# Optimization experiments

Hardware: AMD Instinct MI355X
Metric: run time of the kernel (lower is better)

## Reference

```python
import jax, jax.numpy as jnp
import numpy as np

B, S, D = 2, 2048, 1024
H, HD = 16, 64
WIN = 256


def setup_inputs() -> dict:
    key = jax.random.key(0)
    ks = jax.random.split(key, 9)
    scale = 0.02
    x = jax.random.normal(ks[0], (B, S, D), dtype=jnp.float32)
    Wq = jax.random.normal(ks[1], (D, H * HD), dtype=jnp.float32) * scale
    Wk = jax.random.normal(ks[2], (D, H * HD), dtype=jnp.float32) * scale
    Wv = jax.random.normal(ks[3], (D, H * HD), dtype=jnp.float32) * scale
    Wo = jax.random.normal(ks[4], (H * HD, D), dtype=jnp.float32) * scale
    bq = jnp.zeros((H * HD,), jnp.float32)
    bk = jnp.zeros((H * HD,), jnp.float32)
    bv = jnp.zeros((H * HD,), jnp.float32)
    bo = jnp.zeros((D,), jnp.float32)
    return {"x": x, "Wq": Wq, "bq": bq, "Wk": Wk, "bk": bk,
            "Wv": Wv, "bv": bv, "Wo": Wo, "bo": bo}


def _band_mask(seq_len, window):
    # True where attention is DISALLOWED (matches torch masked positions).
    # mask=None in the original => prefix_size=0, row i attends to
    # j in [max(0, i - window), i]  (causal sliding window).
    i = jnp.arange(seq_len)[:, None]
    j = jnp.arange(seq_len)[None, :]
    return (j > i) | (j < i - window)


def reference(x, Wq, bq, Wk, bk, Wv, bv, Wo, bo):
    b, s, _ = x.shape
    q = (x @ Wq + bq).reshape(b, s, H, HD)
    k = (x @ Wk + bk).reshape(b, s, H, HD)
    v = (x @ Wv + bv).reshape(b, s, H, HD)
    scores = jnp.einsum("bihd,bjhd->bhij", q, k) / jnp.sqrt(jnp.float32(HD))
    mask = _band_mask(s, WIN)  # [s, s], broadcasts over batch, heads
    scores = jnp.where(mask[None, None, :, :], -jnp.inf, scores)
    attn = jax.nn.softmax(scores, axis=-1)  # dropout is identity at eval
    out = jnp.einsum("bhij,bjhd->bihd", attn, v).reshape(b, s, H * HD)
    return out @ Wo + bo
```

## Files before the change

### kernel.cpp

```cpp
#include <hip/hip_runtime.h>
#include <stdint.h>
#include <stddef.h>

#define S_LEN 2048
#define DMODEL 1024
#define NHEAD 16
#define HDIM 64
#define WINSZ 256
#define MROWS 4096
#define NQKV 3072

typedef __bf16 bf16x8 __attribute__((ext_vector_type(8)));
typedef float f32x4 __attribute__((ext_vector_type(4)));
typedef unsigned short us4 __attribute__((ext_vector_type(4)));
typedef unsigned short us8 __attribute__((ext_vector_type(8)));

#define MFMA16(a, b, c) __builtin_amdgcn_mfma_f32_16x16x32_bf16((a), (b), (c), 0, 0, 0)

__device__ __forceinline__ unsigned short f2b(float f) {
  union { float f; unsigned u; } v; v.f = f;
  unsigned u = v.u;
  unsigned r = (u + 0x7FFFu + ((u >> 16) & 1u)) >> 16;
  return (unsigned short)r;
}
__device__ __forceinline__ void storev(float* p, float v) { *p = v; }
__device__ __forceinline__ void storev(unsigned short* p, float v) { *p = f2b(v); }

__device__ __forceinline__ void gload_lds16(const unsigned short* g, unsigned short* l) {
  __builtin_amdgcn_global_load_lds(
      (const __attribute__((address_space(1))) unsigned int*)g,
      (__attribute__((address_space(3))) unsigned int*)l, 16, 0, 0);
}


__global__ void prep_kernel(const float* __restrict__ x,
                            const float* __restrict__ Wq, const float* __restrict__ Wk,
                            const float* __restrict__ Wv, const float* __restrict__ Wo,
                            const float* __restrict__ bq, const float* __restrict__ bk,
                            const float* __restrict__ bv,
                            unsigned short* __restrict__ xb, unsigned short* __restrict__ WqkvT,
                            unsigned short* __restrict__ WoT, float* __restrict__ bqkv) {
  __shared__ float tile[32][33];
  const int bid = blockIdx.x;
  const int tid = threadIdx.x;
  if (bid < 4096) {
    int i = (bid * 256 + tid) * 4;
    float4 v = *reinterpret_cast<const float4*>(x + i);
    us4 o;
    o[0] = f2b(v.x); o[1] = f2b(v.y); o[2] = f2b(v.z); o[3] = f2b(v.w);
    *reinterpret_cast<us4*>(xb + i) = o;
  } else if (bid < 8192) {
    int z = (bid - 4096) >> 10;
    int rem = (bid - 4096) & 1023;
    int bx = rem & 31, by = rem >> 5;
    const float* W = (z == 0) ? Wq : (z == 1) ? Wk : (z == 2) ? Wv : Wo;
    unsigned short* Wt = (z == 3) ? WoT : WqkvT + (size_t)z * DMODEL * DMODEL;
    int n0 = bx * 32, k0 = by * 32;
    int tx = tid & 31, ty = tid >> 5;
#pragma unroll
    for (int i = 0; i < 32; i += 8)
      tile[ty + i][tx] = W[(size_t)(k0 + ty + i) * DMODEL + n0 + tx];
    __syncthreads();
#pragma unroll
    for (int i = 0; i < 32; i += 8)
      Wt[(size_t)(n0 + ty + i) * DMODEL + k0 + tx] = f2b(tile[tx][ty + i]);
  } else {
    int i = (bid - 8192) * 256 + tid;
    if (i < DMODEL) {
      bqkv[i] = bq[i];
      bqkv[DMODEL + i] = bk[i];
      bqkv[2 * DMODEL + i] = bv[i];
    }
  }
}


__global__ __launch_bounds__(512, 2) void gemm8p_kernel(
    const unsigned short* __restrict__ A, const unsigned short* __restrict__ Bt,
    const float* __restrict__ bias, unsigned short* __restrict__ C, int N, int K) {
  __shared__ unsigned short As[2 * 2 * 128 * 64];
  __shared__ unsigned short Bs[2 * 3 * 64 * 64];
  const int tid = threadIdx.x;
  const int cpx = gridDim.x >> 3;
  const int nid = (blockIdx.x & 7) * cpx + (blockIdx.x >> 3);
  const int nbx = N / 192;
  const int by = nid / nbx, bx = nid - by * nbx;
  const int m0 = by * 256, n0 = bx * 192;
  const int wid = tid >> 6, l = tid & 63;
  const int wm = wid >> 2, wn = wid & 3;
  const int lr = l & 15, lg = l >> 4;
  const int srow = tid >> 3;
  const int scol = (tid & 7) * 8;
  const int scol_g = scol ^ (((tid >> 5) & 1) << 4);
  const int NT = K >> 6;

  f32x4 acc[8][3];
#pragma unroll
  for (int i = 0; i < 8; i++)
#pragma unroll
    for (int j = 0; j < 3; j++) acc[i][j] = (f32x4){0.f, 0.f, 0.f, 0.f};

  auto stA = [&](int q, int h, int kt) {
#pragma unroll
    for (int r = 0; r < 2; r++)
      gload_lds16(A + (size_t)(m0 + h * 128 + r * 64 + srow) * K + kt * 64 + scol_g,
                  &As[(((q * 2 + h) * 2 + r) * 64 + srow) * 64 + scol]);
  };
  auto stB = [&](int q, int c, int kt) {
    gload_lds16(Bt + (size_t)(n0 + c * 64 + srow) * K + kt * 64 + scol_g,
                &Bs[((q * 3 + c) * 64 + srow) * 64 + scol]);
  };

  stB(0, 0, 0); stB(0, 1, 0); stB(0, 2, 0); stA(0, 0, 0); stA(0, 1, 0); stB(1, 0, 1);
  asm volatile("s_waitcnt vmcnt(1)" ::: "memory");
  __builtin_amdgcn_s_barrier();

  bf16x8 a[4][2], b01[2][2], b2[2];
  const int colr = (lg * 8) ^ (((lr >> 2) & 1) << 4);
  const int aB = (wm * 128 + lr) * 64 + colr;
  int bOff[3];
#pragma unroll
  for (int j = 0; j < 3; j++) {
    int nrow = wn * 48 + j * 16 + lr;
    bOff[j] = (nrow >> 6) * 4096 + (nrow & 63) * 64 + colr;
  }

#pragma unroll 1
  for (int t = 0; t < NT; t++) {
    const int p = t & 1, q = p ^ 1;
    const int ap = p * 16384, bp = p * 12288;

#pragma unroll
    for (int i = 0; i < 4; i++)
#pragma unroll
      for (int kk = 0; kk < 2; kk++)
        a[i][kk] = *reinterpret_cast<const bf16x8*>(&As[ap + i * 1024 + kk * 32 + aB]);
#pragma unroll
    for (int j = 0; j < 2; j++)
#pragma unroll
      for (int kk = 0; kk < 2; kk++)
        b01[j][kk] = *reinterpret_cast<const bf16x8*>(&Bs[bp + kk * 32 + bOff[j]]);
    if (t + 1 < NT) { stB(q, 1, t + 1); stB(q, 2, t + 1); }
    __builtin_amdgcn_s_barrier();
    __builtin_amdgcn_s_setprio(1);
#pragma unroll
    for (int i = 0; i < 4; i++)
#pragma unroll
      for (int j = 0; j < 2; j++)
#pragma unroll
        for (int kk = 0; kk < 2; kk++)
          acc[i][j] = MFMA16(a[i][kk], b01[j][kk], acc[i][j]);
    __builtin_amdgcn_s_setprio(0);
    __builtin_amdgcn_s_barrier();

#pragma unroll
    for (int kk = 0; kk < 2; kk++)
      b2[kk] = *reinterpret_cast<const bf16x8*>(&Bs[bp + kk * 32 + bOff[2]]);
    if (t + 1 < NT) stA(q, 0, t + 1);
    __builtin_amdgcn_s_barrier();
    __builtin_amdgcn_s_setprio(1);
#pragma unroll
    for (int i = 0; i < 4; i++)
#pragma unroll
      for (int kk = 0; kk < 2; kk++)
        acc[i][2] = MFMA16(a[i][kk], b2[kk], acc[i][2]);
    __builtin_amdgcn_s_setprio(0);
    __builtin_amdgcn_s_barrier();

#pragma unroll
    for (int i = 0; i < 4; i++)
#pragma unroll
      for (int kk = 0; kk < 2; kk++)
        a[i][kk] = *reinterpret_cast<const bf16x8*>(&As[ap + (i + 4) * 1024 + kk * 32 + aB]);
    if (t + 1 < NT) stA(q, 1, t + 1);
    __builtin_amdgcn_s_barrier();
    __builtin_amdgcn_s_setprio(1);
#pragma unroll
    for (int i = 0; i < 4; i++)
#pragma unroll
      for (int j = 0; j < 2; j++)
#pragma unroll
        for (int kk = 0; kk < 2; kk++)
          acc[i + 4][j] = MFMA16(a[i][kk], b01[j][kk], acc[i + 4][j]);
    __builtin_amdgcn_s_setprio(0);
    __builtin_amdgcn_s_barrier();

    if (t + 2 < NT) stB(p, 0, t + 2);
    __builtin_amdgcn_s_barrier();
    __builtin_amdgcn_s_setprio(1);
#pragma unroll
    for (int i = 0; i < 4; i++)
#pragma unroll
      for (int kk = 0; kk < 2; kk++)
        acc[i + 4][2] = MFMA16(a[i][kk], b2[kk], acc[i + 4][2]);
    __builtin_amdgcn_s_setprio(0);
    if (t + 2 < NT) {
      asm volatile("s_waitcnt vmcnt(1)" ::: "memory");
    } else {
      asm volatile("s_waitcnt vmcnt(0)" ::: "memory");
    }
    __builtin_amdgcn_s_barrier();
  }

#pragma unroll
  for (int i = 0; i < 8; i++) {
    int row = m0 + wm * 128 + i * 16 + lg * 4;
#pragma unroll
    for (int j = 0; j < 3; j++) {
      int col = n0 + wn * 48 + j * 16 + lr;
      float bsv = bias[col];
#pragma unroll
      for (int r = 0; r < 4; r++)
        C[(size_t)(row + r) * N + col] = f2b(acc[i][j][r] + bsv);
    }
  }
}


template <typename OutT>
__global__ __launch_bounds__(256, 3) void gemm2p_kernel(
    const unsigned short* __restrict__ A, const unsigned short* __restrict__ Bt,
    const float* __restrict__ bias, OutT* __restrict__ C, int N, int K) {
  __shared__ unsigned short As[2 * 128 * 64];
  __shared__ unsigned short Bs[2 * 64 * 64];
  const int tid = threadIdx.x;
  const int cpx = gridDim.x >> 3;
  const int nid = (blockIdx.x & 7) * cpx + (blockIdx.x >> 3);
  const int nbx = N >> 6;
  const int by = nid / nbx, bx = nid - by * nbx;
  const int m0 = by * 128, n0 = bx * 64;
  const int w = tid >> 6, l = tid & 63;
  const int wm = (w >> 1) * 64, wn = (w & 1) * 32;
  const int lr = l & 15, lg = l >> 4;
  const int srow = tid >> 3;
  const int scol = (tid & 7) * 8;
  const int scol_g = scol ^ (((tid >> 5) & 1) << 4);
  const int NT = K >> 6;

  f32x4 acc[4][2];
#pragma unroll
  for (int i = 0; i < 4; i++)
#pragma unroll
    for (int j = 0; j < 2; j++) acc[i][j] = (f32x4){0.f, 0.f, 0.f, 0.f};

  auto stage = [&](int buf, int kt) {
#pragma unroll
    for (int r = 0; r < 4; r++)
      gload_lds16(A + (size_t)(m0 + r * 32 + srow) * K + kt * 64 + scol_g,
                  &As[(buf * 128 + r * 32 + srow) * 64 + scol]);
#pragma unroll
    for (int r = 0; r < 2; r++)
      gload_lds16(Bt + (size_t)(n0 + r * 32 + srow) * K + kt * 64 + scol_g,
                  &Bs[(buf * 64 + r * 32 + srow) * 64 + scol]);
  };

  stage(0, 0);
  asm volatile("s_waitcnt vmcnt(0)" ::: "memory");
  __builtin_amdgcn_s_barrier();

  const int colr = (lg * 8) ^ (((lr >> 2) & 1) << 4);
  const int aB = (wm + lr) * 64 + colr;
  const int bB = (wn + lr) * 64 + colr;

  int cur = 0;
#pragma unroll 1
  for (int t = 0; t < NT; t++) {
    if (t + 1 < NT) stage(cur ^ 1, t + 1);
    bf16x8 a[4][2], b[2][2];
#pragma unroll
    for (int i = 0; i < 4; i++)
#pragma unroll
      for (int kk = 0; kk < 2; kk++)
        a[i][kk] = *reinterpret_cast<const bf16x8*>(&As[cur * 8192 + i * 1024 + kk * 32 + aB]);
#pragma unroll
    for (int j = 0; j < 2; j++)
#pragma unroll
      for (int kk = 0; kk < 2; kk++)
        b[j][kk] = *reinterpret_cast<const bf16x8*>(&Bs[cur * 4096 + j * 1024 + kk * 32 + bB]);
    __builtin_amdgcn_s_setprio(1);
#pragma unroll
    for (int i = 0; i < 4; i++)
#pragma unroll
      for (int j = 0; j < 2; j++)
#pragma unroll
        for (int kk = 0; kk < 2; kk++)
          acc[i][j] = MFMA16(a[i][kk], b[j][kk], acc[i][j]);
    __builtin_amdgcn_s_setprio(0);
    asm volatile("s_waitcnt vmcnt(0)" ::: "memory");
    __builtin_amdgcn_s_barrier();
    cur ^= 1;
  }

#pragma unroll
  for (int i = 0; i < 4; i++) {
    int row = m0 + wm + i * 16 + lg * 4;
#pragma unroll
    for (int j = 0; j < 2; j++) {
      int col = n0 + wn + j * 16 + lr;
      float bsv = bias[col];
#pragma unroll
      for (int r = 0; r < 4; r++)
        storev(&C[(size_t)(row + r) * N + col], acc[i][j][r] + bsv);
    }
  }
}


__global__ __launch_bounds__(256) void attn_kernel(const unsigned short* __restrict__ qkv,
                                                   unsigned short* __restrict__ attnb) {
  __shared__ unsigned short Ks[64 * 72];
  __shared__ unsigned short Vt[64 * 72];
  __shared__ unsigned short Ps[4][16 * 72];

  const int tid = threadIdx.x;
  const int i0 = blockIdx.x * 64;
  const int h = blockIdx.y;
  const int b = blockIdx.z;
  const int w = tid >> 6, l = tid & 63;
  const int lr = l & 15, lg = l >> 4;
  const size_t rowb = (size_t)b * S_LEN;

  const unsigned short* qptr = qkv + (rowb + i0 + w * 16 + lr) * NQKV + h * HDIM;
  bf16x8 qa[2];
  qa[0] = *reinterpret_cast<const bf16x8*>(qptr + lg * 8);
  qa[1] = *reinterpret_cast<const bf16x8*>(qptr + 32 + lg * 8);

  f32x4 accO[4];
#pragma unroll
  for (int f = 0; f < 4; f++) accO[f] = (f32x4){0.f, 0.f, 0.f, 0.f};
  float Mv[4], Lv[4];
#pragma unroll
  for (int r = 0; r < 4; r++) { Mv[r] = -1e30f; Lv[r] = 0.f; }

  for (int c = 0; c < 5; c++) {
    int j0c = i0 - WINSZ + c * 64;
    if (j0c + 63 < 0) continue;
    __syncthreads();
    {
      int d8 = (tid & 7) * 8;
      int jl0 = tid >> 3;
#pragma unroll
      for (int it = 0; it < 2; it++) {
        int jl = jl0 + it * 32;
        int jg = j0c + jl;
        us8 kv = (us8){0, 0, 0, 0, 0, 0, 0, 0}, vv = (us8){0, 0, 0, 0, 0, 0, 0, 0};
        if (jg >= 0) {
          const unsigned short* kp = qkv + (rowb + jg) * NQKV + DMODEL + h * HDIM + d8;
          kv = *reinterpret_cast<const us8*>(kp);
          vv = *reinterpret_cast<const us8*>(kp + DMODEL);
        }
        *reinterpret_cast<us8*>(&Ks[jl * 72 + d8]) = kv;
#pragma unroll
        for (int e = 0; e < 8; e++) Vt[(d8 + e) * 72 + jl] = vv[e];
      }
    }
    __syncthreads();

    f32x4 sa[4];
#pragma unroll
    for (int f = 0; f < 4; f++) sa[f] = (f32x4){0.f, 0.f, 0.f, 0.f};
#pragma unroll
    for (int f = 0; f < 4; f++) {
      bf16x8 k0v = *reinterpret_cast<const bf16x8*>(&Ks[(f * 16 + lr) * 72 + lg * 8]);
      bf16x8 k1v = *reinterpret_cast<const bf16x8*>(&Ks[(f * 16 + lr) * 72 + 32 + lg * 8]);
      sa[f] = MFMA16(qa[0], k0v, sa[f]);
      sa[f] = MFMA16(qa[1], k1v, sa[f]);
    }
#pragma unroll
    for (int f = 0; f < 4; f++) {
      int jg = j0c + f * 16 + lr;
#pragma unroll
      for (int r = 0; r < 4; r++) {
        int irow = i0 + w * 16 + lg * 4 + r;
        float s = sa[f][r] * 0.125f;
        bool ok = (jg >= 0) && (jg <= irow) && (jg >= irow - WINSZ);
        sa[f][r] = ok ? s : -1e30f;
      }
    }
    float pm[4];
#pragma unroll
    for (int r = 0; r < 4; r++) {
      float m = fmaxf(fmaxf(sa[0][r], sa[1][r]), fmaxf(sa[2][r], sa[3][r]));
#pragma unroll
      for (int off = 1; off < 16; off <<= 1) m = fmaxf(m, __shfl_xor(m, off));
      pm[r] = m;
    }
#pragma unroll
    for (int r = 0; r < 4; r++) {
      float Mn = fmaxf(Mv[r], pm[r]);
      float sc = __expf(Mv[r] - Mn);
      Mv[r] = Mn;
      Lv[r] *= sc;
#pragma unroll
      for (int f = 0; f < 4; f++) accO[f][r] *= sc;
    }
    float rs[4] = {0.f, 0.f, 0.f, 0.f};
#pragma unroll
    for (int f = 0; f < 4; f++) {
#pragma unroll
      for (int r = 0; r < 4; r++) {
        float p = __expf(sa[f][r] - Mv[r]);
        rs[r] += p;
        Ps[w][(lg * 4 + r) * 72 + f * 16 + lr] = f2b(p);
      }
    }
#pragma unroll
    for (int r = 0; r < 4; r++) {
      float s = rs[r];
#pragma unroll
      for (int off = 1; off < 16; off <<= 1) s += __shfl_xor(s, off);
      Lv[r] += s;
    }
    bf16x8 pa0 = *reinterpret_cast<const bf16x8*>(&Ps[w][lr * 72 + lg * 8]);
    bf16x8 pa1 = *reinterpret_cast<const bf16x8*>(&Ps[w][lr * 72 + 32 + lg * 8]);
#pragma unroll
    for (int f = 0; f < 4; f++) {
      bf16x8 v0 = *reinterpret_cast<const bf16x8*>(&Vt[(f * 16 + lr) * 72 + lg * 8]);
      bf16x8 v1 = *reinterpret_cast<const bf16x8*>(&Vt[(f * 16 + lr) * 72 + 32 + lg * 8]);
      accO[f] = MFMA16(pa0, v0, accO[f]);
      accO[f] = MFMA16(pa1, v1, accO[f]);
    }
  }

#pragma unroll
  for (int f = 0; f < 4; f++) {
#pragma unroll
    for (int r = 0; r < 4; r++) {
      float o = accO[f][r] / Lv[r];
      int row = i0 + w * 16 + lg * 4 + r;
      attnb[(rowb + row) * DMODEL + h * HDIM + f * 16 + lr] = f2b(o);
    }
  }
}


extern "C" void kernel_launch(void* const* d_in, const int* in_sizes, int n_in,
                              void* d_out, int out_size, void* d_ws, size_t ws_size,
                              hipStream_t stream) {
  const float* x = (const float*)d_in[0];
  const float* Wq = (const float*)d_in[1];
  const float* bq = (const float*)d_in[2];
  const float* Wk = (const float*)d_in[3];
  const float* bk = (const float*)d_in[4];
  const float* Wv = (const float*)d_in[5];
  const float* bv = (const float*)d_in[6];
  const float* Wo = (const float*)d_in[7];
  const float* bo = (const float*)d_in[8];
  float* out = (float*)d_out;

  unsigned short* xb = (unsigned short*)d_ws;
  unsigned short* WqkvT = xb + (size_t)MROWS * DMODEL;
  unsigned short* WoT = WqkvT + (size_t)3 * DMODEL * DMODEL;
  unsigned short* QKV = WoT + (size_t)DMODEL * DMODEL;
  unsigned short* attnb = QKV + (size_t)MROWS * NQKV;
  float* bqkv = (float*)(attnb + (size_t)MROWS * DMODEL);

  prep_kernel<<<8196, 256, 0, stream>>>(x, Wq, Wk, Wv, Wo, bq, bk, bv,
                                        xb, WqkvT, WoT, bqkv);

  gemm8p_kernel<<<(NQKV / 192) * (MROWS / 256), 512, 0, stream>>>(
      xb, WqkvT, bqkv, QKV, NQKV, DMODEL);

  attn_kernel<<<dim3(S_LEN / 64, NHEAD, 2), 256, 0, stream>>>(QKV, attnb);

  gemm2p_kernel<float><<<(DMODEL / 64) * (MROWS / 128), 256, 0, stream>>>(
      attnb, WoT, bo, out, DMODEL, DMODEL);
}
```

Before: 98.08 us.

## Shrink QKV GEMM tile to 128x192 and simplify to plain double-buffer pipeline

The QKV projection GEMM tile drops from 256x192 to 128x192, which doubles the grid from 256 to 512 blocks and halves the accumulator registers. The launch bound now asks for 4 blocks per SM. The interleaved 8-phase schedule with its staggered B prefetch is replaced by a simple double buffer: prefetch the next k-tile, run all MFMAs, then wait and barrier. This aims for better occupancy and CU fill, but gives up A-tile reuse and the finer-grained overlap of loads with compute.

```diff
diff --git a/kernel.cpp b/kernel.cpp
--- a/kernel.cpp
+++ b/kernel.cpp
@@ -75,17 +75,17 @@
 }
 
 
-__global__ __launch_bounds__(512, 2) void gemm8p_kernel(
+__global__ __launch_bounds__(512, 4) void gemm8p_kernel(
     const unsigned short* __restrict__ A, const unsigned short* __restrict__ Bt,
     const float* __restrict__ bias, unsigned short* __restrict__ C, int N, int K) {
-  __shared__ unsigned short As[2 * 2 * 128 * 64];
-  __shared__ unsigned short Bs[2 * 3 * 64 * 64];
+  __shared__ unsigned short As[2 * 128 * 64];
+  __shared__ unsigned short Bs[2 * 192 * 64];
   const int tid = threadIdx.x;
   const int cpx = gridDim.x >> 3;
   const int nid = (blockIdx.x & 7) * cpx + (blockIdx.x >> 3);
   const int nbx = N / 192;
   const int by = nid / nbx, bx = nid - by * nbx;
-  const int m0 = by * 256, n0 = bx * 192;
+  const int m0 = by * 128, n0 = bx * 192;
   const int wid = tid >> 6, l = tid & 63;
   const int wm = wid >> 2, wn = wid & 3;
   const int lr = l & 15, lg = l >> 4;
@@ -94,117 +94,66 @@
   const int scol_g = scol ^ (((tid >> 5) & 1) << 4);
   const int NT = K >> 6;
 
-  f32x4 acc[8][3];
-#pragma unroll
-  for (int i = 0; i < 8; i++)
+  f32x4 acc[4][3];
+#pragma unroll
+  for (int i = 0; i < 4; i++)
 #pragma unroll
     for (int j = 0; j < 3; j++) acc[i][j] = (f32x4){0.f, 0.f, 0.f, 0.f};
 
-  auto stA = [&](int q, int h, int kt) {
+  auto stage = [&](int buf, int kt) {
 #pragma unroll
     for (int r = 0; r < 2; r++)
-      gload_lds16(A + (size_t)(m0 + h * 128 + r * 64 + srow) * K + kt * 64 + scol_g,
-                  &As[(((q * 2 + h) * 2 + r) * 64 + srow) * 64 + scol]);
+      gload_lds16(A + (size_t)(m0 + r * 64 + srow) * K + kt * 64 + scol_g,
+                  &As[((buf * 2 + r) * 64 + srow) * 64 + scol]);
+#pragma unroll
+    for (int c = 0; c < 3; c++)
+      gload_lds16(Bt + (size_t)(n0 + c * 64 + srow) * K + kt * 64 + scol_g,
+                  &Bs[((buf * 3 + c) * 64 + srow) * 64 + scol]);
   };
-  auto stB = [&](int q, int c, int kt) {
-    gload_lds16(Bt + (size_t)(n0 + c * 64 + srow) * K + kt * 64 + scol_g,
-                &Bs[((q * 3 + c) * 64 + srow) * 64 + scol]);
-  };
-
-  stB(0, 0, 0); stB(0, 1, 0); stB(0, 2, 0); stA(0, 0, 0); stA(0, 1, 0); stB(1, 0, 1);
-  asm volatile("s_waitcnt vmcnt(1)" ::: "memory");
+
+  stage(0, 0);
+  asm volatile("s_waitcnt vmcnt(0)" ::: "memory");
   __builtin_amdgcn_s_barrier();
 
-  bf16x8 a[4][2], b01[2][2], b2[2];
   const int colr = (lg * 8) ^ (((lr >> 2) & 1) << 4);
-  const int aB = (wm * 128 + lr) * 64 + colr;
+  const int aB = (wm * 64 + lr) * 64 + colr;
   int bOff[3];
 #pragma unroll
-  for (int j = 0; j < 3; j++) {
-    int nrow = wn * 48 + j * 16 + lr;
-    bOff[j] = (nrow >> 6) * 4096 + (nrow & 63) * 64 + colr;
-  }
-
+  for (int j = 0; j < 3; j++)
+    bOff[j] = (wn * 48 + j * 16 + lr) * 64 + colr;
+
+  int cur = 0;
 #pragma unroll 1
   for (int t = 0; t < NT; t++) {
-    const int p = t & 1, q = p ^ 1;
-    const int ap = p * 16384, bp = p * 12288;
-
+    if (t + 1 < NT) stage(cur ^ 1, t + 1);
+    bf16x8 a[4][2], b[3][2];
 #pragma unroll
     for (int i = 0; i < 4; i++)
 #pragma unroll
       for (int kk = 0; kk < 2; kk++)
-        a[i][kk] = *reinterpret_cast<const bf16x8*>(&As[ap + i * 1024 + kk * 32 + aB]);
-#pragma unroll
-    for (int j = 0; j < 2; j++)
+        a[i][kk] = *reinterpret_cast<const bf16x8*>(&As[cur * 8192 + i * 1024 + kk * 32 + aB]);
+#pragma unroll
+    for (int j = 0; j < 3; j++)
 #pragma unroll
       for (int kk = 0; kk < 2; kk++)
-        b01[j][kk] = *reinterpret_cast<const bf16x8*>(&Bs[bp + kk * 32 + bOff[j]]);
-    if (t + 1 < NT) { stB(q, 1, t + 1); stB(q, 2, t + 1); }
+        b[j][kk] = *reinterpret_cast<const bf16x8*>(&Bs[cur * 12288 + kk * 32 + bOff[j]]);
+    __builtin_amdgcn_s_setprio(1);
+#pragma unroll
+    for (int i = 0; i < 4; i++)
+#pragma unroll
+      for (int j = 0; j < 3; j++)
+#pragma unroll
+        for (int kk = 0; kk < 2; kk++)
+          acc[i][j] = MFMA16(a[i][kk], b[j][kk], acc[i][j]);
+    __builtin_amdgcn_s_setprio(0);
+    asm volatile("s_waitcnt vmcnt(0)" ::: "memory");
     __builtin_amdgcn_s_barrier();
-    __builtin_amdgcn_s_setprio(1);
-#pragma unroll
-    for (int i = 0; i < 4; i++)
-#pragma unroll
-      for (int j = 0; j < 2; j++)
-#pragma unroll
-        for (int kk = 0; kk < 2; kk++)
-          acc[i][j] = MFMA16(a[i][kk], b01[j][kk], acc[i][j]);
-    __builtin_amdgcn_s_setprio(0);
-    __builtin_amdgcn_s_barrier();
-
-#pragma unroll
-    for (int kk = 0; kk < 2; kk++)
-      b2[kk] = *reinterpret_cast<const bf16x8*>(&Bs[bp + kk * 32 + bOff[2]]);
-    if (t + 1 < NT) stA(q, 0, t + 1);
-    __builtin_amdgcn_s_barrier();
-    __builtin_amdgcn_s_setprio(1);
-#pragma unroll
-    for (int i = 0; i < 4; i++)
-#pragma unroll
-      for (int kk = 0; kk < 2; kk++)
-        acc[i][2] = MFMA16(a[i][kk], b2[kk], acc[i][2]);
-    __builtin_amdgcn_s_setprio(0);
-    __builtin_amdgcn_s_barrier();
-
-#pragma unroll
-    for (int i = 0; i < 4; i++)
-#pragma unroll
-      for (int kk = 0; kk < 2; kk++)
-        a[i][kk] = *reinterpret_cast<const bf16x8*>(&As[ap + (i + 4) * 1024 + kk * 32 + aB]);
-    if (t + 1 < NT) stA(q, 1, t + 1);
-    __builtin_amdgcn_s_barrier();
-    __builtin_amdgcn_s_setprio(1);
-#pragma unroll
-    for (int i = 0; i < 4; i++)
-#pragma unroll
-      for (int j = 0; j < 2; j++)
-#pragma unroll
-        for (int kk = 0; kk < 2; kk++)
-          acc[i + 4][j] = MFMA16(a[i][kk], b01[j][kk], acc[i + 4][j]);
-    __builtin_amdgcn_s_setprio(0);
-    __builtin_amdgcn_s_barrier();
-
-    if (t + 2 < NT) stB(p, 0, t + 2);
-    __builtin_amdgcn_s_barrier();
-    __builtin_amdgcn_s_setprio(1);
-#pragma unroll
-    for (int i = 0; i < 4; i++)
-#pragma unroll
-      for (int kk = 0; kk < 2; kk++)
-        acc[i + 4][2] = MFMA16(a[i][kk], b2[kk], acc[i + 4][2]);
-    __builtin_amdgcn_s_setprio(0);
-    if (t + 2 < NT) {
-      asm volatile("s_waitcnt vmcnt(1)" ::: "memory");
-    } else {
-      asm volatile("s_waitcnt vmcnt(0)" ::: "memory");
-    }
-    __builtin_amdgcn_s_barrier();
-  }
-
-#pragma unroll
-  for (int i = 0; i < 8; i++) {
-    int row = m0 + wm * 128 + i * 16 + lg * 4;
+    cur ^= 1;
+  }
+
+#pragma unroll
+  for (int i = 0; i < 4; i++) {
+    int row = m0 + wm * 64 + i * 16 + lg * 4;
 #pragma unroll
     for (int j = 0; j < 3; j++) {
       int col = n0 + wn * 48 + j * 16 + lr;
@@ -458,7 +407,7 @@
   prep_kernel<<<8196, 256, 0, stream>>>(x, Wq, Wk, Wv, Wo, bq, bk, bv,
                                         xb, WqkvT, WoT, bqkv);
 
-  gemm8p_kernel<<<(NQKV / 192) * (MROWS / 256), 512, 0, stream>>>(
+  gemm8p_kernel<<<(NQKV / 192) * (MROWS / 128), 512, 0, stream>>>(
       xb, WqkvT, bqkv, QKV, NQKV, DMODEL);
 
   attn_kernel<<<dim3(S_LEN / 64, NHEAD, 2), 256, 0, stream>>>(QKV, attnb);
```

New measurement: 90.23 us. -8.0%, faster.
